# Kernel optimization log

Hardware: AMD Instinct MI355X
Metric: run time of the kernel (lower is better)

## Reference

```python
import jax, jax.numpy as jnp
import numpy as np

TOPK = 13
NUM_CLASSES = 80
ALPHA = 1.0
BETA = 3.0
EPS = 1e-9
K_NEAR = 4
N_BINS = 36  # theta bins: arange(0, 360, 10)


def _dist_max_per_bin(anc_points, gt_pts):
    """gt_pts: (bs,nm,360,2), anc_points: (na,2) -> (bs,nm,na,36) ray targets."""
    d = gt_pts[:, :, None, :, :] - anc_points[None, None, :, None, :]  # (bs,nm,na,360,2)
    dist = jnp.sqrt(jnp.sum(d * d, axis=-1))                           # (bs,nm,na,360)
    ang = jnp.rad2deg(jnp.arctan2(d[..., 1], d[..., 0])) % 360.0       # (bs,nm,na,360)
    theta = jnp.arange(0, 360, 360 // N_BINS).astype(ang.dtype)        # (36,)

    def per_theta(th):
        diff = jnp.abs(ang - th)
        diff = jnp.where(diff > 180.0, 360.0 - diff, diff)
        neg_v, idx = jax.lax.top_k(-diff, K_NEAR)   # 4 nearest-angle contour pts
        val = -neg_v
        dk = jnp.take_along_axis(dist, idx, axis=-1)
        dk = jnp.where(jnp.min(val, axis=-1, keepdims=True) > 3.0, 1e-6, dk)
        return jnp.max(dk, axis=-1)                 # (bs,nm,na)

    dm = jax.lax.map(per_theta, theta)              # (36,bs,nm,na); chunked to bound memory
    return jnp.maximum(jnp.moveaxis(dm, 0, -1), 1e-6)


def _mask_iou(target, pred):
    l_max = jnp.maximum(target, pred)
    l_min = jnp.maximum(jnp.minimum(target, pred), 1e-6)
    return jnp.sum(l_min, -1) / jnp.sum(l_max, -1)


def _forward(pd_scores, pd_bboxes, anc_points, gt_labels, gt_bboxes, mask_gt, gt_coor):
    bs, na, nc = pd_scores.shape
    nm = gt_bboxes.shape[1]
    gl = gt_labels[..., 0]            # (bs,nm) int
    mgt = mask_gt[..., 0]             # (bs,nm) float
    gt_pts = gt_coor.reshape(bs, nm, 360, 2)

    # select_candidates_in_gts: anchor center strictly inside gt box
    lt, rb = gt_bboxes[..., :2], gt_bboxes[..., 2:]
    deltas = jnp.concatenate([anc_points[None, None] - lt[:, :, None],
                              rb[:, :, None] - anc_points[None, None]], axis=-1)
    mask_in_gts = (jnp.min(deltas, -1) > 1e-9).astype(pd_scores.dtype)  # (bs,nm,na)
    mask_sel = (mask_in_gts * mgt[:, :, None]) > 0

    # get_box_metrics_polar (dense over (bs,nm,na) instead of boolean-mask select)
    dist_max = _dist_max_per_bin(anc_points, gt_pts)                    # (bs,nm,na,36)
    overlaps = jnp.where(mask_sel, _mask_iou(dist_max, pd_bboxes[:, None]), 0.0)
    bbox_scores = jnp.take_along_axis(jnp.swapaxes(pd_scores, 1, 2), gl[:, :, None], axis=1)
    bbox_scores = jnp.where(mask_sel, bbox_scores, 0.0)
    align_metric = (bbox_scores ** ALPHA) * (overlaps ** BETA)

    # select_topk_candidates
    _, topk_idxs = jax.lax.top_k(align_metric, TOPK)
    topk_idxs = jnp.where(mgt[:, :, None] > 0, topk_idxs, 0)
    count = jnp.sum(jax.nn.one_hot(topk_idxs, na, dtype=align_metric.dtype), axis=-2)
    mask_topk = jnp.where(count > 1, 0.0, count)
    mask_pos = mask_topk * mask_in_gts * mgt[:, :, None]

    # select_highest_overlaps
    fg = jnp.sum(mask_pos, -2)                                          # (bs,na)
    multi = fg[:, None, :] > 1
    is_max = jnp.moveaxis(jax.nn.one_hot(jnp.argmax(overlaps, 1), nm, dtype=mask_pos.dtype), -1, 1)
    mask_pos = jnp.where(multi, is_max, mask_pos)
    fg_mask = jnp.sum(mask_pos, -2)
    target_gt_idx = jnp.argmax(mask_pos, -2)                            # (bs,na)

    # per-positive ray-distance targets + polar centerness (dense, masked)
    mask_pos_b = mask_pos > 0
    gt_dist = jnp.where(mask_pos_b[..., None], dist_max, 0.0)           # (bs,nm,na,36)
    cent = jnp.sqrt(jnp.min(dist_max, -1) / jnp.max(dist_max, -1))
    centerness_gt = jnp.where(mask_pos_b, cent, 0.0)                    # (bs,nm,na)

    # get_targets
    target_labels = jnp.maximum(jnp.take_along_axis(gl, target_gt_idx, axis=1), 0)
    target_bboxes = jnp.take_along_axis(gt_bboxes, target_gt_idx[..., None], axis=1)
    target_scores = jax.nn.one_hot(target_labels, NUM_CLASSES, dtype=pd_scores.dtype)
    target_scores = jnp.where((fg_mask > 0)[..., None], target_scores, 0.0)

    am = align_metric * mask_pos
    pos_align = jnp.max(am, -1, keepdims=True)
    pos_ov = jnp.max(overlaps * mask_pos, -1, keepdims=True)
    norm_align = jnp.max(am * pos_ov / (pos_align + EPS), -2)[..., None]  # (bs,na,1)
    target_scores = target_scores * norm_align

    return (target_labels, target_bboxes, target_scores, mask_pos_b,
            target_gt_idx, gt_dist, centerness_gt, fg_mask > 0)


def setup_inputs():
    key = jax.random.key(0)
    k = jax.random.split(key, 6)
    bs, nc, nm = 2, 80, 10
    pts, strs = [], []
    for s in (8, 16, 32):  # 640x640 YOLO grid -> 8400 anchors
        n = 640 // s
        yv, xv = np.meshgrid(np.arange(n), np.arange(n), indexing='ij')
        pts.append(np.stack([(xv + 0.5) * s, (yv + 0.5) * s], -1).reshape(-1, 2))
        strs.append(np.full((pts[-1].shape[0], 1), s, dtype=np.float32))
    anc_points = jnp.asarray(np.concatenate(pts).astype(np.float32))
    stride_tensor = jnp.asarray(np.concatenate(strs))
    na = anc_points.shape[0]
    pd_scores = jax.random.uniform(k[0], (bs, na, nc), dtype=jnp.float32)
    pd_bboxes = jax.random.uniform(k[1], (bs, na, 36), dtype=jnp.float32) * 100.0 + 1.0
    gt_labels = jax.random.randint(k[2], (bs, nm, 1), 0, nc)
    ctr = jax.random.uniform(k[3], (bs, nm, 2), dtype=jnp.float32) * 440.0 + 100.0
    wh = jax.random.uniform(k[4], (bs, nm, 2), dtype=jnp.float32) * 140.0 + 40.0
    gt_bboxes = jnp.concatenate([ctr - wh / 2.0, ctr + wh / 2.0], -1)
    th = jnp.arange(360.0) * (jnp.pi / 180.0)
    rad = (jnp.min(wh, -1, keepdims=True) / 2.0) * (0.6 + 0.4 * jax.random.uniform(k[5], (bs, nm, 360), dtype=jnp.float32))
    ray = jnp.stack([jnp.cos(th), jnp.sin(th)], -1)  # (360,2)
    gt_coor = (ctr[:, :, None, :] + rad[..., None] * ray[None, None]).reshape(bs, nm, 720)
    mask_gt = jnp.ones((bs, nm, 1), dtype=jnp.float32).at[1, 7:].set(0.0)
    return dict(pd_scores=pd_scores, pd_bboxes=pd_bboxes, anc_points=anc_points,
                gt_labels=gt_labels, gt_bboxes=gt_bboxes, mask_gt=mask_gt,
                gt_coor=gt_coor, stride_tensor=stride_tensor, ss=640,
                gt_center=ctr, imgsz=640)


def reference(pd_scores, pd_bboxes, anc_points, gt_labels, gt_bboxes, mask_gt, gt_coor, stride_tensor, ss, gt_center, imgsz):
    # ss, gt_center, imgsz, stride_tensor are accepted (as in the torch signature) but unused
    return _forward(pd_scores, pd_bboxes, anc_points, gt_labels, gt_bboxes, mask_gt, gt_coor)
```

## Files before the change

### kernel.cpp

```cpp
#include <hip/hip_runtime.h>

#define BS 2
#define NM 10
#define NA 8400
#define NC 80
#define NBIN 36
#define KTOP 13
#define NRECT (BS*NM*3)

__device__ __forceinline__ void rect_one(int bm, int lv,
    const float* __restrict__ gtb, const float* __restrict__ mgt,
    int& x0, int& y0, int& cx, int& cnt, int& n, int& base){
  cnt = 0; x0 = 0; y0 = 0; cx = 0; n = 0; base = 0;
  if (mgt[bm] > 0.f){
    float s = (float)(8 << lv);
    n = 640 >> (3 + lv);
    base = (lv == 0) ? 0 : ((lv == 1) ? 6400 : 8000);
    float lx = gtb[bm*4+0], ly = gtb[bm*4+1];
    float rx = gtb[bm*4+2], ry = gtb[bm*4+3];
    int a0 = (int)ceilf(lx/s - 0.5f); a0 = min(max(a0, 0), n);
    while (a0 > 0   &&  (((a0-1)+0.5f)*s - lx > 1e-9f)) a0--;
    while (a0 < n   && !(((a0  )+0.5f)*s - lx > 1e-9f)) a0++;
    int a1 = (int)floorf(rx/s - 0.5f); a1 = min(max(a1, -1), n-1);
    while (a1 < n-1 &&  (rx - ((a1+1)+0.5f)*s > 1e-9f)) a1++;
    while (a1 >= 0  && !(rx - ((a1  )+0.5f)*s > 1e-9f)) a1--;
    int b0 = (int)ceilf(ly/s - 0.5f); b0 = min(max(b0, 0), n);
    while (b0 > 0   &&  (((b0-1)+0.5f)*s - ly > 1e-9f)) b0--;
    while (b0 < n   && !(((b0  )+0.5f)*s - ly > 1e-9f)) b0++;
    int b1 = (int)floorf(ry/s - 0.5f); b1 = min(max(b1, -1), n-1);
    while (b1 < n-1 &&  (ry - ((b1+1)+0.5f)*s > 1e-9f)) b1++;
    while (b1 >= 0  && !(ry - ((b1  )+0.5f)*s > 1e-9f)) b1--;
    cx = max(0, a1 - a0 + 1);
    int cy = max(0, b1 - b0 + 1);
    cnt = cx * cy;
    x0 = a0; y0 = b0;
  }
}

__device__ __forceinline__ void rect_setup(int tid,
    const float* __restrict__ gtb, const float* __restrict__ mgt,
    int* sx0, int* sy0, int* scx, int* scum, int* sn, int* sbase){
  if (tid < NRECT){
    int bm = tid/3, lv = tid - bm*3;
    int x0, y0, cx, cnt, n, base;
    rect_one(bm, lv, gtb, mgt, x0, y0, cx, cnt, n, base);
    sx0[tid] = x0; sy0[tid] = y0; scx[tid] = cx;
    scum[tid] = cnt; sn[tid] = n; sbase[tid] = base;
  }
  __syncthreads();
  if (tid == 0){
    int acc = 0;
    for (int r = 0; r < NRECT; r++){ int c = scum[r]; scum[r] = acc; acc += c; }
    scum[NRECT] = acc;
  }
  __syncthreads();
}

__device__ __forceinline__ int pair_from_p(int p,
    const int* sx0, const int* sy0, const int* scx,
    const int* scum, const int* sn, const int* sbase){
  int r = 0;
  while (r < NRECT-1 && scum[r+1] <= p) r++;
  int idx = p - scum[r];
  int cx = scx[r];
  int yi = idx / cx;
  int xi = idx - yi*cx;
  int a = sbase[r] + (sy0[r] + yi)*sn[r] + (sx0[r] + xi);
  int bm = r/3;
  return bm*NA + a;
}

__device__ __forceinline__ bool in_pair(int t,
    const float* __restrict__ anc, const float* __restrict__ gtb,
    const float* __restrict__ mgt){
  int a = t % NA; int bm = t / NA;
  if (mgt[bm] <= 0.f) return false;
  float ax = anc[2*a], ay = anc[2*a+1];
  float lx = gtb[bm*4+0], ly = gtb[bm*4+1];
  float rx = gtb[bm*4+2], ry = gtb[bm*4+3];
  float mind = fminf(fminf(ax-lx, ay-ly), fminf(rx-ax, ry-ay));
  return (mind > 1e-9f);
}

__global__ __launch_bounds__(256)
void k_dist(const float* __restrict__ pds, const float* __restrict__ pdb,
            const float* __restrict__ anc, const int* __restrict__ gl,
            const float* __restrict__ gtb, const float* __restrict__ mgt,
            const float* __restrict__ coor,
            float* __restrict__ out, float* __restrict__ wf){
  float* o_scores  = out + 84000;
  float* o_gtdist  = out + 1612800;
  float* o_cent    = out + 7660800;
  float* w_align = wf + 16;
  float* w_ovl   = w_align + BS*NM*NA;
  float* w_mask  = w_ovl + BS*NM*NA;
  float* w_pa    = w_mask + BS*NM*NA;

  __shared__ int sx0[NRECT], sy0[NRECT], scx[NRECT], scum[NRECT+1], sn[NRECT], sbase[NRECT];
  __shared__ float2 s_da[360];
  __shared__ float  s_m[NBIN*33];

  int tid = threadIdx.x;
  int lane = tid & 63, wave = tid >> 6;
  int gsz  = gridDim.x * 256;
  int gtid = blockIdx.x * 256 + tid;

  rect_setup(tid, gtb, mgt, sx0, sy0, scx, scum, sn, sbase);
  int total = scum[NRECT];

  {
    float4 z = make_float4(0.f, 0.f, 0.f, 0.f);
    float4* sc4 = (float4*)o_scores;
    for (int i = gtid; i < (BS*NA*NC)/4; i += gsz) sc4[i] = z;
    float4* ce4 = (float4*)o_cent;
    for (int i = gtid; i < (BS*NM*NA)/4; i += gsz) ce4[i] = z;
    if (gtid < 2*BS*NM) w_pa[gtid] = 0.f;
    for (int t = gtid; t < BS*NM*NA; t += gsz){
      w_mask[t] = 0.f;
      if (!in_pair(t, anc, gtb, mgt)){
        w_align[t] = 0.f;
        w_ovl[t]   = 0.f;
      }
    }
    float4* gd4 = (float4*)o_gtdist;
    for (int i = gtid; i < (BS*NM*NA*NBIN)/4; i += gsz){
      int t = i / 9;
      if (!in_pair(t, anc, gtb, mgt)) gd4[i] = z;
    }
  }

  for (int p = blockIdx.x; p < total; p += gridDim.x){
    int t = pair_from_p(p, sx0, sy0, scx, scum, sn, sbase);
    int a = t % NA; int bm = t / NA; int b = bm / NM;
    float ax = anc[2*a], ay = anc[2*a+1];
    const float* cc = coor + bm*720;
    for (int i = tid; i < 360; i += 256){
      float dx = cc[2*i]   - ax;
      float dy = cc[2*i+1] - ay;
      float dist = sqrtf(dx*dx + dy*dy);
      float an = atan2f(dy, dx) * 57.29577951308232f;
      if (an < 0.f) an += 360.f;
      s_da[i] = make_float2(dist, an);
    }
    __syncthreads();
    if (lane < NBIN){
      float th = (float)(lane*10);
      float v0=1e30f, v1=1e30f, v2=1e30f, v3=1e30f;
      float d0=0.f, d1=0.f, d2=0.f, d3=0.f;
      int base = wave*90;
      for (int k = 0; k < 90; k++){
        float2 da = s_da[base + k];
        float diff = fabsf(da.y - th);
        diff = fminf(diff, 360.f - diff);
        if (diff < v3){
          v3 = diff; d3 = da.x;
          if (v3 < v2){ float tv=v2; v2=v3; v3=tv; float td=d2; d2=d3; d3=td; }
          if (v2 < v1){ float tv=v1; v1=v2; v2=tv; float td=d1; d1=d2; d2=td; }
          if (v1 < v0){ float tv=v0; v0=v1; v1=tv; float td=d0; d0=d1; d1=td; }
        }
      }
      int mb = lane*33 + wave*8;
      s_m[mb+0]=v0; s_m[mb+1]=v1; s_m[mb+2]=v2; s_m[mb+3]=v3;
      s_m[mb+4]=d0; s_m[mb+5]=d1; s_m[mb+6]=d2; s_m[mb+7]=d3;
    }
    __syncthreads();
    if (wave == 0){
      float sum_min = 0.f, sum_max = 0.f;
      if (lane < NBIN){
        int mb = lane*33;
        float h0=s_m[mb+0], h1=s_m[mb+8], h2=s_m[mb+16], h3=s_m[mb+24];
        int p0=0, p1=0, p2=0, p3=0;
        float v0m = 0.f, dmax = 0.f;
#pragma unroll
        for (int step = 0; step < 4; step++){
          float bv = h0; int bw = 0;
          if (h1 < bv){ bv = h1; bw = 1; }
          if (h2 < bv){ bv = h2; bw = 2; }
          if (h3 < bv){ bv = h3; bw = 3; }
          float dd;
          if (bw == 0){ dd = s_m[mb+4+p0]; p0++; h0 = (p0<4)? s_m[mb+p0]    : 1e30f; }
          else if (bw == 1){ dd = s_m[mb+12+p1]; p1++; h1 = (p1<4)? s_m[mb+8+p1]  : 1e30f; }
          else if (bw == 2){ dd = s_m[mb+20+p2]; p2++; h2 = (p2<4)? s_m[mb+16+p2] : 1e30f; }
          else             { dd = s_m[mb+28+p3]; p3++; h3 = (p3<4)? s_m[mb+24+p3] : 1e30f; }
          if (step == 0) v0m = bv;
          dmax = fmaxf(dmax, dd);
        }
        float dm = (v0m > 3.0f) ? 1e-6f : dmax;
        float dfin = fmaxf(dm, 1e-6f);
        o_gtdist[(size_t)t*NBIN + lane] = dfin;
        float pr = pdb[((size_t)b*NA + a)*NBIN + lane];
        sum_max = fmaxf(dfin, pr);
        sum_min = fmaxf(fminf(dfin, pr), 1e-6f);
      }
      for (int off = 32; off > 0; off >>= 1){
        sum_min += __shfl_down(sum_min, off);
        sum_max += __shfl_down(sum_max, off);
      }
      if (lane == 0){
        float ov = sum_min / sum_max;
        int cls = gl[bm];
        float sc = pds[((size_t)b*NA + a)*NC + cls];
        w_align[t] = sc * ov * ov * ov;
        w_ovl[t]   = ov;
      }
    }
    __syncthreads();
  }
}

__global__ __launch_bounds__(256)
void k_topk(const float* __restrict__ gtb, const float* __restrict__ mgt,
            const float* __restrict__ w_align, float* __restrict__ w_mask){
  int bm = blockIdx.x;
  const float* al = w_align + (size_t)bm*NA;
  int tid = threadIdx.x;
  __shared__ int rx0[3], ry0[3], rcx[3], rcum[4], rn[3], rbase[3];
  __shared__ float sv[256*KTOP];
  __shared__ int   si[256*KTOP];
  __shared__ float wv4[4];
  __shared__ int   wi4[4];

  if (tid < 3){
    int x0, y0, cx, cnt, n, base;
    rect_one(bm, tid, gtb, mgt, x0, y0, cx, cnt, n, base);
    rx0[tid]=x0; ry0[tid]=y0; rcx[tid]=cx; rcum[tid]=cnt; rn[tid]=n; rbase[tid]=base;
  }
  __syncthreads();
  if (tid == 0){
    int acc = 0;
#pragma unroll
    for (int r = 0; r < 3; r++){ int c = rcum[r]; rcum[r] = acc; acc += c; }
    rcum[3] = acc;
  }
  __syncthreads();
  int total = rcum[3];

  float v[KTOP]; int ix[KTOP];
#pragma unroll
  for (int j = 0; j < KTOP; j++){ v[j] = -1.f; ix[j] = 0x7fffffff; }
  for (int p = tid; p < total; p += 256){
    int r = (p >= rcum[1]) + (p >= rcum[2]);
    int idx = p - rcum[r];
    int cx = rcx[r];
    int yi = idx / cx;
    int xi = idx - yi*cx;
    int a = rbase[r] + (ry0[r] + yi)*rn[r] + (rx0[r] + xi);
    float x = al[a];
    if (x > v[KTOP-1]){
      v[KTOP-1] = x; ix[KTOP-1] = a;
#pragma unroll
      for (int j = KTOP-1; j > 0; j--){
        if (v[j] > v[j-1]){
          float tv = v[j-1]; v[j-1] = v[j]; v[j] = tv;
          int   ti = ix[j-1]; ix[j-1] = ix[j]; ix[j] = ti;
        }
      }
    }
  }
#pragma unroll
  for (int j = 0; j < KTOP; j++){ sv[tid*KTOP+j] = v[j]; si[tid*KTOP+j] = ix[j]; }

  int head = 0;
  int lane = tid & 63, wave = tid >> 6;
  for (int r = 0; r < KTOP; r++){
    float cv = sv[tid*KTOP + head];
    int   ci = si[tid*KTOP + head];
    float rv = cv; int ri = ci;
    for (int off = 32; off > 0; off >>= 1){
      float ov = __shfl_down(rv, off);
      int   oi = __shfl_down(ri, off);
      if (ov > rv || (ov == rv && oi < ri)){ rv = ov; ri = oi; }
    }
    if (lane == 0){ wv4[wave] = rv; wi4[wave] = ri; }
    __syncthreads();
    float Wv = wv4[0]; int Wi = wi4[0];
#pragma unroll
    for (int w = 1; w < 4; w++){
      float ov = wv4[w]; int oi = wi4[w];
      if (ov > Wv || (ov == Wv && oi < Wi)){ Wv = ov; Wi = oi; }
    }
    if (ci == Wi && head < KTOP-1) head++;
    if (tid == 0 && Wv > 0.f) w_mask[(size_t)bm*NA + Wi] = 1.f;
    __syncthreads();
  }
}

__global__ void k_final(const float* __restrict__ w_align, const float* __restrict__ w_ovl,
                        float* __restrict__ w_mask,
                        const int* __restrict__ gl, const float* __restrict__ gtb,
                        float* __restrict__ o_labels, float* __restrict__ o_bboxes,
                        float* __restrict__ o_maskpos, float* __restrict__ o_gtidx,
                        float* __restrict__ o_fg,
                        float* __restrict__ w_pa, float* __restrict__ w_po){
  int t = blockIdx.x*256 + threadIdx.x;
  if (t >= BS*NA) return;
  int a = t % NA, b = t / NA;
  float mp[NM];
  int fg = 0;
#pragma unroll
  for (int m = 0; m < NM; m++){
    mp[m] = w_mask[((size_t)(b*NM+m))*NA + a];
    fg += (mp[m] > 0.f) ? 1 : 0;
  }
  if (fg > 1){
    float bv = -1.f; int bi = 0;
#pragma unroll
    for (int m = 0; m < NM; m++){
      float v = w_ovl[((size_t)(b*NM+m))*NA + a];
      if (v > bv){ bv = v; bi = m; }
    }
#pragma unroll
    for (int m = 0; m < NM; m++){
      mp[m] = (m == bi) ? 1.f : 0.f;
      w_mask[((size_t)(b*NM+m))*NA + a] = mp[m];
    }
    fg = 1;
  }
  int tgt = 0;
#pragma unroll
  for (int m = NM-1; m >= 0; m--) if (mp[m] > 0.f) tgt = m;
#pragma unroll
  for (int m = 0; m < NM; m++) o_maskpos[((size_t)(b*NM+m))*NA + a] = mp[m];
  o_gtidx[t] = (float)tgt;
  o_fg[t] = (fg > 0) ? 1.f : 0.f;
  int lbl = gl[b*NM + tgt]; if (lbl < 0) lbl = 0;
  o_labels[t] = (float)lbl;
  const float* bx = gtb + (b*NM + tgt)*4;
  ((float4*)o_bboxes)[t] = make_float4(bx[0], bx[1], bx[2], bx[3]);
  if (fg > 0){
    int bmx = b*NM + tgt;
    float av  = w_align[(size_t)bmx*NA + a];
    float ovv = w_ovl[(size_t)bmx*NA + a];
    atomicMax((unsigned int*)&w_pa[bmx], __float_as_uint(av));
    atomicMax((unsigned int*)&w_po[bmx], __float_as_uint(ovv));
  }
}

#define NB_FIX 512
__global__ void k_fuse(const float* __restrict__ gtb, const float* __restrict__ mgt,
                       const float* __restrict__ w_mask, float* __restrict__ o_gtdist,
                       float* __restrict__ o_cent,
                       const float* __restrict__ w_align,
                       const float* __restrict__ w_pa, const float* __restrict__ w_po,
                       const float* __restrict__ o_labels, const float* __restrict__ o_fg,
                       const float* __restrict__ o_gtidx, float* __restrict__ o_scores){
  if (blockIdx.x < NB_FIX){
    __shared__ int sx0[NRECT], sy0[NRECT], scx[NRECT], scum[NRECT+1], sn[NRECT], sbase[NRECT];
    int tid = threadIdx.x;
    rect_setup(tid, gtb, mgt, sx0, sy0, scx, scum, sn, sbase);
    int total = scum[NRECT];
    int lane = tid & 63, wave = tid >> 6;
    for (int p = blockIdx.x*4 + wave; p < total; p += NB_FIX*4){
      int t = pair_from_p(p, sx0, sy0, scx, scum, sn, sbase);
      float m = w_mask[t];
      float* row = o_gtdist + (size_t)t*NBIN;
      if (m > 0.f){
        float vmin = 1e30f, vmax = 0.f;
        if (lane < NBIN){
          float v = row[lane];
          vmin = v; vmax = v;
        }
        for (int off = 32; off > 0; off >>= 1){
          vmin = fminf(vmin, __shfl_down(vmin, off));
          vmax = fmaxf(vmax, __shfl_down(vmax, off));
        }
        if (lane == 0) o_cent[t] = sqrtf(vmin / vmax);
      } else {
        if (lane < NBIN) row[lane] = 0.f;
      }
    }
  } else {
    int t = (blockIdx.x - NB_FIX)*256 + threadIdx.x;
    if (t < BS*NA && o_fg[t] > 0.f){
      int a = t % NA, b = t / NA;
      int m = (int)o_gtidx[t];
      int bm = b*NM + m;
      float av = w_align[(size_t)bm*NA + a];
      float norm = av * w_po[bm] / (w_pa[bm] + 1e-9f);
      int lbl = (int)o_labels[t];
      o_scores[(size_t)t*NC + lbl] = norm;
    }
  }
}

extern "C" void kernel_launch(void* const* d_in, const int* in_sizes, int n_in,
                              void* d_out, int out_size, void* d_ws, size_t ws_size,
                              hipStream_t stream){
  const float* pds  = (const float*)d_in[0];
  const float* pdb  = (const float*)d_in[1];
  const float* anc  = (const float*)d_in[2];
  const int*   gl   = (const int*)  d_in[3];
  const float* gtb  = (const float*)d_in[4];
  const float* mgt  = (const float*)d_in[5];
  const float* coor = (const float*)d_in[6];

  float* out = (float*)d_out;
  float* o_labels  = out;
  float* o_bboxes  = o_labels + BS*NA;
  float* o_scores  = o_bboxes + BS*NA*4;
  float* o_maskpos = o_scores + (size_t)BS*NA*NC;
  float* o_gtidx   = o_maskpos + BS*NM*NA;
  float* o_gtdist  = o_gtidx + BS*NA;
  float* o_cent    = o_gtdist + (size_t)BS*NM*NA*NBIN;
  float* o_fg      = o_cent + BS*NM*NA;

  float* wf      = (float*)d_ws;
  float* w_align = wf + 16;
  float* w_ovl   = w_align + BS*NM*NA;
  float* w_mask  = w_ovl + BS*NM*NA;
  float* w_pa    = w_mask + BS*NM*NA;
  float* w_po    = w_pa + BS*NM;

  k_dist<<<4096, 256, 0, stream>>>(pds, pdb, anc, gl, gtb, mgt, coor, out, wf);
  k_topk<<<BS*NM, 256, 0, stream>>>(gtb, mgt, w_align, w_mask);
  k_final<<<(BS*NA+255)/256, 256, 0, stream>>>(w_align, w_ovl, w_mask, gl, gtb,
                                               o_labels, o_bboxes, o_maskpos, o_gtidx, o_fg,
                                               w_pa, w_po);
  k_fuse<<<NB_FIX + (BS*NA+255)/256, 256, 0, stream>>>(gtb, mgt, w_mask,
                                                       o_gtdist, o_cent,
                                                       w_align, w_pa, w_po,
                                                       o_labels, o_fg, o_gtidx, o_scores);
}
```

Baseline: 181.8 us.

## Bucket contour points by angle per wave to replace brute-force nearest-angle scan

Each wave now processes one anchor-gt pair independently, with no block-level barriers. Within a wave, the 360 contour points are bucket-sorted into 36 angular bins using a shared-memory count, a prefix scan and a scatter. Each theta lane then scans only its neighbouring buckets, widening the search only when the current 4th-nearest candidate could still be beaten. Candidates are ranked by a packed (diff, index) 64-bit key, which breaks ties by index as top_k does. This removes the 360×36 comparison work and the per-pair block syncs, at the cost of shared-memory atomics, wave-divergent bucket lengths and a grid halved to 2048 blocks.

```diff
diff --git a/kernel.cpp b/kernel.cpp
--- a/kernel.cpp
+++ b/kernel.cpp
@@ -82,6 +82,27 @@
   return (mind > 1e-9f);
 }
 
+__device__ __forceinline__ void scan_bucket(const float2* __restrict__ so,
+    int st, int len, int kmax, float th,
+    unsigned long long& k0, unsigned long long& k1,
+    unsigned long long& k2, unsigned long long& k3){
+  for (int k = 0; k < kmax; k++){
+    bool pr = (k < len);
+    float2 e = so[pr ? (st + k) : 0];
+    float ad = fabsf(e.x - th);
+    float diff = fminf(ad, 360.f - ad);
+    unsigned long long key =
+      ((unsigned long long)__float_as_uint(diff) << 32) |
+      (unsigned int)__float_as_uint(e.y);
+    if (pr && key < k3){
+      k3 = key;
+      if (k3 < k2){ unsigned long long tt=k2; k2=k3; k3=tt; }
+      if (k2 < k1){ unsigned long long tt=k1; k1=k2; k2=tt; }
+      if (k1 < k0){ unsigned long long tt=k0; k0=k1; k1=tt; }
+    }
+  }
+}
+
 __global__ __launch_bounds__(256)
 void k_dist(const float* __restrict__ pds, const float* __restrict__ pdb,
             const float* __restrict__ anc, const int* __restrict__ gl,
@@ -97,8 +118,11 @@
   float* w_pa    = w_mask + BS*NM*NA;
 
   __shared__ int sx0[NRECT], sy0[NRECT], scx[NRECT], scum[NRECT+1], sn[NRECT], sbase[NRECT];
-  __shared__ float2 s_da[360];
-  __shared__ float  s_m[NBIN*33];
+  __shared__ float2 s_da[4][360];
+  __shared__ float2 s_so[4][360];
+  __shared__ int s_cnt[4][NBIN];
+  __shared__ int s_off[4][NBIN];
+  __shared__ int s_pos[4][NBIN];
 
   int tid = threadIdx.x;
   int lane = tid & 63, wave = tid >> 6;
@@ -129,82 +153,115 @@
     }
   }
 
-  for (int p = blockIdx.x; p < total; p += gridDim.x){
+  const unsigned long long KMAX = ~0ull;
+  bool active = (lane < NBIN);
+  int nwaves = gridDim.x * 4;
+  for (int p = blockIdx.x*4 + wave; p < total; p += nwaves){
     int t = pair_from_p(p, sx0, sy0, scx, scum, sn, sbase);
     int a = t % NA; int bm = t / NA; int b = bm / NM;
     float ax = anc[2*a], ay = anc[2*a+1];
     const float* cc = coor + bm*720;
-    for (int i = tid; i < 360; i += 256){
-      float dx = cc[2*i]   - ax;
-      float dy = cc[2*i+1] - ay;
-      float dist = sqrtf(dx*dx + dy*dy);
-      float an = atan2f(dy, dx) * 57.29577951308232f;
-      if (an < 0.f) an += 360.f;
-      s_da[i] = make_float2(dist, an);
-    }
-    __syncthreads();
-    if (lane < NBIN){
-      float th = (float)(lane*10);
-      float v0=1e30f, v1=1e30f, v2=1e30f, v3=1e30f;
-      float d0=0.f, d1=0.f, d2=0.f, d3=0.f;
-      int base = wave*90;
-      for (int k = 0; k < 90; k++){
-        float2 da = s_da[base + k];
-        float diff = fabsf(da.y - th);
-        diff = fminf(diff, 360.f - diff);
-        if (diff < v3){
-          v3 = diff; d3 = da.x;
-          if (v3 < v2){ float tv=v2; v2=v3; v3=tv; float td=d2; d2=d3; d3=td; }
-          if (v2 < v1){ float tv=v1; v1=v2; v2=tv; float td=d1; d1=d2; d2=td; }
-          if (v1 < v0){ float tv=v0; v0=v1; v1=tv; float td=d0; d0=d1; d1=td; }
-        }
-      }
-      int mb = lane*33 + wave*8;
-      s_m[mb+0]=v0; s_m[mb+1]=v1; s_m[mb+2]=v2; s_m[mb+3]=v3;
-      s_m[mb+4]=d0; s_m[mb+5]=d1; s_m[mb+6]=d2; s_m[mb+7]=d3;
-    }
-    __syncthreads();
-    if (wave == 0){
-      float sum_min = 0.f, sum_max = 0.f;
-      if (lane < NBIN){
-        int mb = lane*33;
-        float h0=s_m[mb+0], h1=s_m[mb+8], h2=s_m[mb+16], h3=s_m[mb+24];
-        int p0=0, p1=0, p2=0, p3=0;
-        float v0m = 0.f, dmax = 0.f;
-#pragma unroll
-        for (int step = 0; step < 4; step++){
-          float bv = h0; int bw = 0;
-          if (h1 < bv){ bv = h1; bw = 1; }
-          if (h2 < bv){ bv = h2; bw = 2; }
-          if (h3 < bv){ bv = h3; bw = 3; }
-          float dd;
-          if (bw == 0){ dd = s_m[mb+4+p0]; p0++; h0 = (p0<4)? s_m[mb+p0]    : 1e30f; }
-          else if (bw == 1){ dd = s_m[mb+12+p1]; p1++; h1 = (p1<4)? s_m[mb+8+p1]  : 1e30f; }
-          else if (bw == 2){ dd = s_m[mb+20+p2]; p2++; h2 = (p2<4)? s_m[mb+16+p2] : 1e30f; }
-          else             { dd = s_m[mb+28+p3]; p3++; h3 = (p3<4)? s_m[mb+24+p3] : 1e30f; }
-          if (step == 0) v0m = bv;
-          dmax = fmaxf(dmax, dd);
-        }
-        float dm = (v0m > 3.0f) ? 1e-6f : dmax;
-        float dfin = fmaxf(dm, 1e-6f);
-        o_gtdist[(size_t)t*NBIN + lane] = dfin;
-        float pr = pdb[((size_t)b*NA + a)*NBIN + lane];
-        sum_max = fmaxf(dfin, pr);
-        sum_min = fmaxf(fminf(dfin, pr), 1e-6f);
-      }
-      for (int off = 32; off > 0; off >>= 1){
-        sum_min += __shfl_down(sum_min, off);
-        sum_max += __shfl_down(sum_max, off);
-      }
-      if (lane == 0){
-        float ov = sum_min / sum_max;
-        int cls = gl[bm];
-        float sc = pds[((size_t)b*NA + a)*NC + cls];
-        w_align[t] = sc * ov * ov * ov;
-        w_ovl[t]   = ov;
-      }
-    }
-    __syncthreads();
+
+    if (active) s_cnt[wave][lane] = 0;
+    __threadfence_block();
+
+    float angr[6]; int bktr[6];
+#pragma unroll
+    for (int c = 0; c < 6; c++){
+      int i = lane + c*64;
+      bktr[c] = -1;
+      if (i < 360){
+        float dx = cc[2*i]   - ax;
+        float dy = cc[2*i+1] - ay;
+        float dist = sqrtf(dx*dx + dy*dy);
+        float an = atan2f(dy, dx) * 57.29577951308232f;
+        if (an < 0.f) an += 360.f;
+        s_da[wave][i] = make_float2(dist, an);
+        int bkt = (int)(an*0.1f + 0.5f); if (bkt >= NBIN) bkt -= NBIN;
+        angr[c] = an; bktr[c] = bkt;
+        atomicAdd(&s_cnt[wave][bkt], 1);
+      }
+    }
+    __threadfence_block();
+
+    int myc = active ? s_cnt[wave][lane] : 0;
+    int v = myc;
+    for (int off = 1; off < 64; off <<= 1){
+      int o = __shfl_up(v, off);
+      if (lane >= off) v += o;
+    }
+    if (active){ s_off[wave][lane] = v - myc; s_pos[wave][lane] = v - myc; }
+    int km = myc;
+    for (int off = 32; off > 0; off >>= 1){
+      int o = __shfl_xor(km, off);
+      km = (o > km) ? o : km;
+    }
+    __threadfence_block();
+
+#pragma unroll
+    for (int c = 0; c < 6; c++){
+      if (bktr[c] >= 0){
+        int slot = atomicAdd(&s_pos[wave][bktr[c]], 1);
+        s_so[wave][slot] = make_float2(angr[c], __int_as_float(lane + c*64));
+      }
+    }
+    __threadfence_block();
+
+    unsigned long long k0 = KMAX, k1 = KMAX, k2 = KMAX, k3 = KMAX;
+    float th = (float)(lane*10);
+    for (int j = 0; j < 3; j++){
+      int q = (lane + NBIN - 1 + j) % NBIN;
+      int st = s_off[wave][q];
+      int len = active ? s_cnt[wave][q] : 0;
+      scan_bucket(&s_so[wave][0], st, len, km, th, k0, k1, k2, k3);
+    }
+    if (active){
+      int wext = 2;
+      while (wext <= 18){
+        float diff3 = __uint_as_float((unsigned int)(k3 >> 32));
+        if (diff3 < (float)(10*wext - 5) - 0.01f) break;
+        int qa = (lane + wext) % NBIN;
+        int qb = (lane + NBIN - wext) % NBIN;
+        scan_bucket(&s_so[wave][0], s_off[wave][qa], s_cnt[wave][qa],
+                    s_cnt[wave][qa], th, k0, k1, k2, k3);
+        if (qb != qa)
+          scan_bucket(&s_so[wave][0], s_off[wave][qb], s_cnt[wave][qb],
+                      s_cnt[wave][qb], th, k0, k1, k2, k3);
+        wext++;
+      }
+    }
+
+    float sum_min = 0.f, sum_max = 0.f;
+    if (active){
+      float diff0 = __uint_as_float((unsigned int)(k0 >> 32));
+      float dm;
+      if (diff0 > 3.0f) dm = 1e-6f;
+      else {
+        int i0 = (int)(unsigned int)(k0 & 0xffffffffull);
+        int i1 = (int)(unsigned int)(k1 & 0xffffffffull);
+        int i2 = (int)(unsigned int)(k2 & 0xffffffffull);
+        int i3 = (int)(unsigned int)(k3 & 0xffffffffull);
+        dm = fmaxf(fmaxf(s_da[wave][i0].x, s_da[wave][i1].x),
+                   fmaxf(s_da[wave][i2].x, s_da[wave][i3].x));
+      }
+      float dfin = fmaxf(dm, 1e-6f);
+      o_gtdist[(size_t)t*NBIN + lane] = dfin;
+      float pr = pdb[((size_t)b*NA + a)*NBIN + lane];
+      sum_max = fmaxf(dfin, pr);
+      sum_min = fmaxf(fminf(dfin, pr), 1e-6f);
+    }
+    for (int off = 32; off > 0; off >>= 1){
+      sum_min += __shfl_down(sum_min, off);
+      sum_max += __shfl_down(sum_max, off);
+    }
+    if (lane == 0){
+      float ov = sum_min / sum_max;
+      int cls = gl[bm];
+      float sc = pds[((size_t)b*NA + a)*NC + cls];
+      w_align[t] = sc * ov * ov * ov;
+      w_ovl[t]   = ov;
+    }
+    __threadfence_block();
   }
 }
 
@@ -411,7 +468,7 @@
   float* w_pa    = w_mask + BS*NM*NA;
   float* w_po    = w_pa + BS*NM;
 
-  k_dist<<<4096, 256, 0, stream>>>(pds, pdb, anc, gl, gtb, mgt, coor, out, wf);
+  k_dist<<<2048, 256, 0, stream>>>(pds, pdb, anc, gl, gtb, mgt, coor, out, wf);
   k_topk<<<BS*NM, 256, 0, stream>>>(gtb, mgt, w_align, w_mask);
   k_final<<<(BS*NA+255)/256, 256, 0, stream>>>(w_align, w_ovl, w_mask, gl, gtb,
                                                o_labels, o_bboxes, o_maskpos, o_gtidx, o_fg,
```

After: 442.7 us. 143% more time.

## Split zero-fill into separate kernel and spread angle scan over six chunks

Applied to the files above, without the earlier changes.

Zero-initialisation of scores, gt-distance, centre and workspace buffers moves out of k_dist into a new k_zero kernel. It now clears everything unconditionally with float4 stores instead of running per-element in_pair checks. The per-pair nearest-angle scan now uses 216 threads (36 bins × 6 chunks of 60 points) instead of 4 waves × 36 lanes over 90 points, and the merge step combines six sorted lists. This shortens the serial scan per pair and removes branchy init work, at the cost of an extra kernel launch and writing the full gt-distance buffer before it is partly overwritten.

```diff
diff --git a/kernel.cpp b/kernel.cpp
--- a/kernel.cpp
+++ b/kernel.cpp
@@ -70,16 +70,15 @@
   return bm*NA + a;
 }
 
-__device__ __forceinline__ bool in_pair(int t,
-    const float* __restrict__ anc, const float* __restrict__ gtb,
-    const float* __restrict__ mgt){
-  int a = t % NA; int bm = t / NA;
-  if (mgt[bm] <= 0.f) return false;
-  float ax = anc[2*a], ay = anc[2*a+1];
-  float lx = gtb[bm*4+0], ly = gtb[bm*4+1];
-  float rx = gtb[bm*4+2], ry = gtb[bm*4+3];
-  float mind = fminf(fminf(ax-lx, ay-ly), fminf(rx-ax, ry-ay));
-  return (mind > 1e-9f);
+__global__ void k_zero(float* __restrict__ out, float* __restrict__ wf){
+  float4 z = make_float4(0.f,0.f,0.f,0.f);
+  int gsz = gridDim.x*256, gtid = blockIdx.x*256 + threadIdx.x;
+  float4* a = (float4*)(out + 84000);
+  for (int i = gtid; i < 1344000/4; i += gsz) a[i] = z;
+  float4* b = (float4*)(out + 1612800);
+  for (int i = gtid; i < (6048000+168000)/4; i += gsz) b[i] = z;
+  float4* c = (float4*)(wf + 16);
+  for (int i = gtid; i < (3*BS*NM*NA + 40)/4; i += gsz) c[i] = z;
 }
 
 __global__ __launch_bounds__(256)
@@ -88,46 +87,25 @@
             const float* __restrict__ gtb, const float* __restrict__ mgt,
             const float* __restrict__ coor,
             float* __restrict__ out, float* __restrict__ wf){
-  float* o_scores  = out + 84000;
   float* o_gtdist  = out + 1612800;
-  float* o_cent    = out + 7660800;
   float* w_align = wf + 16;
   float* w_ovl   = w_align + BS*NM*NA;
-  float* w_mask  = w_ovl + BS*NM*NA;
-  float* w_pa    = w_mask + BS*NM*NA;
 
   __shared__ int sx0[NRECT], sy0[NRECT], scx[NRECT], scum[NRECT+1], sn[NRECT], sbase[NRECT];
   __shared__ float2 s_da[360];
-  __shared__ float  s_m[NBIN*33];
+  __shared__ float  s_m[NBIN*49];
 
   int tid = threadIdx.x;
   int lane = tid & 63, wave = tid >> 6;
-  int gsz  = gridDim.x * 256;
-  int gtid = blockIdx.x * 256 + tid;
 
   rect_setup(tid, gtb, mgt, sx0, sy0, scx, scum, sn, sbase);
   int total = scum[NRECT];
 
-  {
-    float4 z = make_float4(0.f, 0.f, 0.f, 0.f);
-    float4* sc4 = (float4*)o_scores;
-    for (int i = gtid; i < (BS*NA*NC)/4; i += gsz) sc4[i] = z;
-    float4* ce4 = (float4*)o_cent;
-    for (int i = gtid; i < (BS*NM*NA)/4; i += gsz) ce4[i] = z;
-    if (gtid < 2*BS*NM) w_pa[gtid] = 0.f;
-    for (int t = gtid; t < BS*NM*NA; t += gsz){
-      w_mask[t] = 0.f;
-      if (!in_pair(t, anc, gtb, mgt)){
-        w_align[t] = 0.f;
-        w_ovl[t]   = 0.f;
-      }
-    }
-    float4* gd4 = (float4*)o_gtdist;
-    for (int i = gtid; i < (BS*NM*NA*NBIN)/4; i += gsz){
-      int t = i / 9;
-      if (!in_pair(t, anc, gtb, mgt)) gd4[i] = z;
-    }
-  }
+  int id = tid;
+  int bin = id % 36;
+  int chunk = id / 36;
+  bool act = (id < 216);
+  float th = (float)(bin*10);
 
   for (int p = blockIdx.x; p < total; p += gridDim.x){
     int t = pair_from_p(p, sx0, sy0, scx, scum, sn, sbase);
@@ -143,12 +121,11 @@
       s_da[i] = make_float2(dist, an);
     }
     __syncthreads();
-    if (lane < NBIN){
-      float th = (float)(lane*10);
+    if (act){
       float v0=1e30f, v1=1e30f, v2=1e30f, v3=1e30f;
       float d0=0.f, d1=0.f, d2=0.f, d3=0.f;
-      int base = wave*90;
-      for (int k = 0; k < 90; k++){
+      int base = chunk*60;
+      for (int k = 0; k < 60; k++){
         float2 da = s_da[base + k];
         float diff = fabsf(da.y - th);
         diff = fminf(diff, 360.f - diff);
@@ -159,7 +136,7 @@
           if (v1 < v0){ float tv=v0; v0=v1; v1=tv; float td=d0; d0=d1; d1=td; }
         }
       }
-      int mb = lane*33 + wave*8;
+      int mb = bin*49 + chunk*8;
       s_m[mb+0]=v0; s_m[mb+1]=v1; s_m[mb+2]=v2; s_m[mb+3]=v3;
       s_m[mb+4]=d0; s_m[mb+5]=d1; s_m[mb+6]=d2; s_m[mb+7]=d3;
     }
@@ -167,9 +144,10 @@
     if (wave == 0){
       float sum_min = 0.f, sum_max = 0.f;
       if (lane < NBIN){
-        int mb = lane*33;
-        float h0=s_m[mb+0], h1=s_m[mb+8], h2=s_m[mb+16], h3=s_m[mb+24];
-        int p0=0, p1=0, p2=0, p3=0;
+        int mb = lane*49;
+        float h0=s_m[mb+0], h1=s_m[mb+8],  h2=s_m[mb+16],
+              h3=s_m[mb+24], h4=s_m[mb+32], h5=s_m[mb+40];
+        int p0=0, p1=0, p2=0, p3=0, p4=0, p5=0;
         float v0m = 0.f, dmax = 0.f;
 #pragma unroll
         for (int step = 0; step < 4; step++){
@@ -177,11 +155,15 @@
           if (h1 < bv){ bv = h1; bw = 1; }
           if (h2 < bv){ bv = h2; bw = 2; }
           if (h3 < bv){ bv = h3; bw = 3; }
+          if (h4 < bv){ bv = h4; bw = 4; }
+          if (h5 < bv){ bv = h5; bw = 5; }
           float dd;
-          if (bw == 0){ dd = s_m[mb+4+p0]; p0++; h0 = (p0<4)? s_m[mb+p0]    : 1e30f; }
-          else if (bw == 1){ dd = s_m[mb+12+p1]; p1++; h1 = (p1<4)? s_m[mb+8+p1]  : 1e30f; }
+          if (bw == 0){ dd = s_m[mb+ 4+p0]; p0++; h0 = (p0<4)? s_m[mb   +p0] : 1e30f; }
+          else if (bw == 1){ dd = s_m[mb+12+p1]; p1++; h1 = (p1<4)? s_m[mb+ 8+p1] : 1e30f; }
           else if (bw == 2){ dd = s_m[mb+20+p2]; p2++; h2 = (p2<4)? s_m[mb+16+p2] : 1e30f; }
-          else             { dd = s_m[mb+28+p3]; p3++; h3 = (p3<4)? s_m[mb+24+p3] : 1e30f; }
+          else if (bw == 3){ dd = s_m[mb+28+p3]; p3++; h3 = (p3<4)? s_m[mb+24+p3] : 1e30f; }
+          else if (bw == 4){ dd = s_m[mb+36+p4]; p4++; h4 = (p4<4)? s_m[mb+32+p4] : 1e30f; }
+          else             { dd = s_m[mb+44+p5]; p5++; h5 = (p5<4)? s_m[mb+40+p5] : 1e30f; }
           if (step == 0) v0m = bv;
           dmax = fmaxf(dmax, dd);
         }
@@ -411,6 +393,7 @@
   float* w_pa    = w_mask + BS*NM*NA;
   float* w_po    = w_pa + BS*NM;
 
+  k_zero<<<2048, 256, 0, stream>>>(out, wf);
   k_dist<<<4096, 256, 0, stream>>>(pds, pdb, anc, gl, gtb, mgt, coor, out, wf);
   k_topk<<<BS*NM, 256, 0, stream>>>(gtb, mgt, w_align, w_mask);
   k_final<<<(BS*NA+255)/256, 256, 0, stream>>>(w_align, w_ovl, w_mask, gl, gtb,
```

Measured after the change: 169.7 us. 6.7% less time.
